# Kernel optimization log

Hardware: AMD Instinct MI355X
Metric: run time of the kernel (lower is better)

## Reference

```python
import jax, jax.numpy as jnp
import numpy as np

NEG_INF = -1e30

def setup_inputs() -> dict:
    key = jax.random.key(0)
    k1, k2, k3 = jax.random.split(key, 3)
    B, H, S, D = 2, 16, 2048, 128
    q = jax.random.normal(k1, (B, H, S, D), dtype=jnp.float32)
    k = jax.random.normal(k2, (B, H, S, D), dtype=jnp.float32)
    v = jax.random.normal(k3, (B, H, S, D), dtype=jnp.float32)
    return {"q": q, "k": k, "v": v}

def reference(q, k, v):
    # F.scaled_dot_product_attention(q, k, v, is_causal=True), MATH backend:
    # full score matrix, causal mask (top-left aligned: j <= i), softmax, bmm.
    D = q.shape[-1]
    scale = 1.0 / jnp.sqrt(jnp.asarray(D, dtype=q.dtype))
    scores = jnp.einsum('bhqd,bhkd->bhqk', q, k) * scale  # [B,H,S,S]
    Sq, Sk = scores.shape[-2], scores.shape[-1]
    causal = jnp.arange(Sk)[None, :] <= jnp.arange(Sq)[:, None]  # [Sq,Sk]
    scores = jnp.where(causal[None, None], scores, NEG_INF)
    attn = jax.nn.softmax(scores, axis=-1)
    return jnp.einsum('bhqk,bhkd->bhqd', attn, v)
```

## Files before the change

### kernel.cpp

```cpp
#include <hip/hip_runtime.h>
#include <cstdint>
#include <cstddef>

typedef __attribute__((ext_vector_type(8))) short short8;
typedef __attribute__((ext_vector_type(4))) float floatx4;
typedef __attribute__((ext_vector_type(2))) unsigned int uint2v;

namespace {
constexpr int kBH  = 32;
constexpr int kS   = 2048;
constexpr int kD   = 128;
constexpr int kBQ  = 64;
constexpr int kBK  = 64;
constexpr int kNQT = kS / kBQ;
constexpr int PST  = 72;
constexpr size_t kKVElems = (size_t)kBH * kS * kD;
}

__device__ __forceinline__ unsigned short f32_bf16(float f) {
    union { float f; unsigned u; } c; c.f = f;
    unsigned u = c.u;
    u += 0x7FFFu + ((u >> 16) & 1u);
    return (unsigned short)(u >> 16);
}

__device__ __forceinline__ unsigned pack_bf16x2(float lo, float hi) {
    return (unsigned)f32_bf16(lo) | ((unsigned)f32_bf16(hi) << 16);
}

__device__ __forceinline__ void gl_lds16(const void* g, void* l) {
    __builtin_amdgcn_global_load_lds(
        (const __attribute__((address_space(1))) unsigned int*)g,
        (__attribute__((address_space(3))) unsigned int*)l, 16, 0, 0);
}

__global__ __launch_bounds__(256)
void prepass(const float* __restrict__ K, const float* __restrict__ V,
             unsigned short* __restrict__ Kb, unsigned short* __restrict__ Vt) {
    const int b = (int)blockIdx.x;
    const int t = (int)threadIdx.x;
    if (b < 4096) {
        const size_t i0 = ((size_t)b * 256 + t) * 8;
        floatx4 a = *(const floatx4*)(K + i0);
        floatx4 c = *(const floatx4*)(K + i0 + 4);
        union { unsigned short us[8]; short8 v; } pk;
#pragma unroll
        for (int i = 0; i < 4; ++i) { pk.us[i] = f32_bf16(a[i]); pk.us[4 + i] = f32_bf16(c[i]); }
        *(short8*)(Kb + i0) = pk.v;
    } else {
        __shared__ float ldsT[64][68];
        const int vb = b - 4096;
        const int bh = vb >> 6;
        const int rem = vb & 63;
        const int s0 = (rem >> 1) * 64;
        const int d0 = (rem & 1) * 64;
        const float* vbase = V + ((size_t)bh * kS + s0) * kD + d0;
        const int sr = t >> 4, c4 = (t & 15) * 4;
#pragma unroll
        for (int p = 0; p < 4; ++p) {
            const int s = p * 16 + sr;
            *(floatx4*)&ldsT[s][c4] = *(const floatx4*)(vbase + (size_t)s * kD + c4);
        }
        __syncthreads();
        const int dr = t >> 2, sc = (t & 3) * 16;
        union { unsigned short us[16]; short8 v[2]; } pk;
#pragma unroll
        for (int j = 0; j < 16; ++j) pk.us[j] = f32_bf16(ldsT[sc + j][dr]);
        unsigned short* out = Vt + ((size_t)(bh * kD + d0 + dr)) * kS + s0 + sc;
        *(short8*)out = pk.v[0];
        *(short8*)(out + 8) = pk.v[1];
    }
}


struct TileState {
    short8  qf[4];
    floatx4 oacc[8];
    float   lsum[4];
};

__device__ __forceinline__ void tile_step(
    TileState& ts, const unsigned short* kT, const unsigned short* vT,
    unsigned short* pw, int l16, int quad, int rowl, bool doMask)
{
    floatx4 sacc[4];
#pragma unroll
    for (int nt = 0; nt < 4; ++nt) {
        floatx4 acc = (floatx4){0.f, 0.f, 0.f, 0.f};
#pragma unroll
        for (int ks = 0; ks < 4; ++ks) {
            short8 kf = *(const short8*)&kT[(nt * 16 + l16) * 128 + (((ks * 4 + quad) ^ l16) << 3)];
            acc = __builtin_amdgcn_mfma_f32_16x16x32_bf16(ts.qf[ks], kf, acc, 0, 0, 0);
        }
        sacc[nt] = acc;
    }

    if (doMask) {
#pragma unroll
        for (int nt = 0; nt < 4; ++nt) {
            const int col = nt * 16 + l16;
#pragma unroll
            for (int r = 0; r < 4; ++r)
                if (col > rowl + r) sacc[nt][r] = -1e30f;
        }
    }

#pragma unroll
    for (int nt = 0; nt < 4; ++nt)
#pragma unroll
        for (int r = 0; r < 4; ++r)
            sacc[nt][r] = __expf(sacc[nt][r]);
#pragma unroll
    for (int r = 0; r < 4; ++r)
        ts.lsum[r] += (sacc[0][r] + sacc[1][r]) + (sacc[2][r] + sacc[3][r]);

#pragma unroll
    for (int nt = 0; nt < 4; ++nt)
#pragma unroll
        for (int r = 0; r < 4; ++r)
            pw[(quad * 4 + r) * PST + nt * 16 + l16] = f32_bf16(sacc[nt][r]);

    short8 pf[2];
#pragma unroll
    for (int ks = 0; ks < 2; ++ks)
        pf[ks] = *(const short8*)&pw[l16 * PST + ks * 32 + quad * 8];

#pragma unroll
    for (int nd = 0; nd < 8; ++nd) {
        floatx4 acc = ts.oacc[nd];
#pragma unroll
        for (int ks = 0; ks < 2; ++ks) {
            short8 vf = *(const short8*)&vT[(nd * 16 + l16) * 64 + ((((ks * 4 + quad)) ^ (l16 & 7)) << 3)];
            acc = __builtin_amdgcn_mfma_f32_16x16x32_bf16(pf[ks], vf, acc, 0, 0, 0);
        }
        ts.oacc[nd] = acc;
    }
}

__global__ __launch_bounds__(256, 2)
void fa_fwd_ws(const float* __restrict__ Qg, const unsigned short* __restrict__ Kb,
               const unsigned short* __restrict__ Vt, float* __restrict__ Og) {
    const int id = (int)blockIdx.x;
    const int qA = id >> 5;
    const int qB = kNQT - 1 - qA;
    const int bh = id & (kBH - 1);
    const int t    = (int)threadIdx.x;
    const int wave = t >> 6;
    const int lane = t & 63;
    const int quad = lane >> 4;
    const int l16  = lane & 15;
    const int rowl = wave * 16 + quad * 4;

    __shared__ __align__(16) unsigned short kT0[kBK * 128];
    __shared__ __align__(16) unsigned short kT1[kBK * 128];
    __shared__ __align__(16) unsigned short vT0[kD * 64];
    __shared__ __align__(16) unsigned short vT1[kD * 64];
    __shared__ __align__(16) unsigned short pT[4 * 16 * PST];
    unsigned short* pw = &pT[wave * 16 * PST];

    const float scale = 0.08838834764831845f;

    TileState A, B;
#pragma unroll
    for (int i = 0; i < 8; ++i) { A.oacc[i] = (floatx4){0,0,0,0}; B.oacc[i] = (floatx4){0,0,0,0}; }
#pragma unroll
    for (int r = 0; r < 4; ++r) { A.lsum[r] = 0.f; B.lsum[r] = 0.f; }

    {
        const float* qpA = Qg + ((size_t)bh * kS + qA * kBQ + wave * 16 + l16) * kD;
        const float* qpB = Qg + ((size_t)bh * kS + qB * kBQ + wave * 16 + l16) * kD;
#pragma unroll
        for (int ks = 0; ks < 4; ++ks) {
            const int d0 = ks * 32 + quad * 8;
            floatx4 a0 = *(const floatx4*)(qpA + d0);
            floatx4 a1 = *(const floatx4*)(qpA + d0 + 4);
            floatx4 b0 = *(const floatx4*)(qpB + d0);
            floatx4 b1 = *(const floatx4*)(qpB + d0 + 4);
            union { unsigned short us[8]; short8 v; } pa, pb;
#pragma unroll
            for (int i = 0; i < 4; ++i) {
                pa.us[i]     = f32_bf16(a0[i] * scale);
                pa.us[4 + i] = f32_bf16(a1[i] * scale);
                pb.us[i]     = f32_bf16(b0[i] * scale);
                pb.us[4 + i] = f32_bf16(b1[i] * scale);
            }
            A.qf[ks] = pa.v;
            B.qf[ks] = pb.v;
        }
    }

    const unsigned short* kBase = Kb + (size_t)bh * kS * kD;
    const unsigned short* vBase = Vt + (size_t)bh * kD * kS;

    auto stage = [&](int kt, unsigned short* kDst, unsigned short* vDst) {
        const int kj0 = kt * kBK;
        const int rbase = wave * 16;
#pragma unroll
        for (int i = 0; i < 4; ++i) {
            const int row = rbase + i * 4 + (lane >> 4);
            const int cg  = (lane & 15) ^ (row & 15);
            gl_lds16(kBase + ((size_t)(kj0 + row)) * kD + cg * 8,
                     &kDst[(rbase + i * 4) * 128]);
        }
        const int dbase = wave * 32;
#pragma unroll
        for (int i = 0; i < 4; ++i) {
            const int d  = dbase + i * 8 + (lane >> 3);
            const int cg = (lane & 7) ^ (d & 7);
            gl_lds16(vBase + (size_t)d * kS + kj0 + cg * 8,
                     &vDst[(dbase + i * 8) * 64]);
        }
    };

    const int last = qB;
    stage(0, kT0, vT0);
    __syncthreads();

    int kt = 0;
    for (;;) {
        if (kt < last) stage(kt + 1, kT1, vT1);
        if (kt <= qA) tile_step(A, kT0, vT0, pw, l16, quad, rowl, kt == qA);
        tile_step(B, kT0, vT0, pw, l16, quad, rowl, kt == last);
        __syncthreads();
        if (kt == last) break;
        ++kt;
        if (kt < last) stage(kt + 1, kT0, vT0);
        if (kt <= qA) tile_step(A, kT1, vT1, pw, l16, quad, rowl, kt == qA);
        tile_step(B, kT1, vT1, pw, l16, quad, rowl, kt == last);
        __syncthreads();
        if (kt == last) break;
        ++kt;
    }

#pragma unroll
    for (int tile = 0; tile < 2; ++tile) {
        TileState& ts = tile ? B : A;
        const int qt = tile ? qB : qA;
        float ls[4];
#pragma unroll
        for (int r = 0; r < 4; ++r) ls[r] = ts.lsum[r];
#pragma unroll
        for (int off = 1; off < 16; off <<= 1)
#pragma unroll
            for (int r = 0; r < 4; ++r)
                ls[r] += __shfl_xor(ls[r], off, 64);
        float inv[4];
#pragma unroll
        for (int r = 0; r < 4; ++r) inv[r] = 1.0f / ls[r];
        float* ob = Og + ((size_t)bh * kS + qt * kBQ + wave * 16 + quad * 4) * kD;
#pragma unroll
        for (int nd = 0; nd < 8; ++nd)
#pragma unroll
            for (int r = 0; r < 4; ++r)
                ob[(size_t)r * kD + nd * 16 + l16] = ts.oacc[nd][r] * inv[r];
    }
}

namespace {
constexpr int KSTf = 136;
constexpr int VSTf = 72;
}

__device__ __forceinline__ void tile_step_f(
    TileState& ts, const unsigned short* kT, const unsigned short* vT,
    unsigned short* pw, int l16, int quad, int rowl, bool doMask)
{
    floatx4 sacc[4];
#pragma unroll
    for (int nt = 0; nt < 4; ++nt) {
        floatx4 acc = (floatx4){0.f, 0.f, 0.f, 0.f};
#pragma unroll
        for (int ks = 0; ks < 4; ++ks) {
            short8 kf = *(const short8*)&kT[(nt * 16 + l16) * KSTf + ks * 32 + quad * 8];
            acc = __builtin_amdgcn_mfma_f32_16x16x32_bf16(ts.qf[ks], kf, acc, 0, 0, 0);
        }
        sacc[nt] = acc;
    }
    if (doMask) {
#pragma unroll
        for (int nt = 0; nt < 4; ++nt) {
            const int col = nt * 16 + l16;
#pragma unroll
            for (int r = 0; r < 4; ++r)
                if (col > rowl + r) sacc[nt][r] = -1e30f;
        }
    }
#pragma unroll
    for (int nt = 0; nt < 4; ++nt)
#pragma unroll
        for (int r = 0; r < 4; ++r)
            sacc[nt][r] = __expf(sacc[nt][r]);
#pragma unroll
    for (int r = 0; r < 4; ++r)
        ts.lsum[r] += (sacc[0][r] + sacc[1][r]) + (sacc[2][r] + sacc[3][r]);
#pragma unroll
    for (int nt = 0; nt < 4; ++nt)
#pragma unroll
        for (int r = 0; r < 4; ++r)
            pw[(quad * 4 + r) * PST + nt * 16 + l16] = f32_bf16(sacc[nt][r]);
    short8 pf[2];
#pragma unroll
    for (int ks = 0; ks < 2; ++ks)
        pf[ks] = *(const short8*)&pw[l16 * PST + ks * 32 + quad * 8];
#pragma unroll
    for (int nd = 0; nd < 8; ++nd) {
        floatx4 acc = ts.oacc[nd];
#pragma unroll
        for (int ks = 0; ks < 2; ++ks) {
            short8 vf = *(const short8*)&vT[(nd * 16 + l16) * VSTf + ks * 32 + quad * 8];
            acc = __builtin_amdgcn_mfma_f32_16x16x32_bf16(pf[ks], vf, acc, 0, 0, 0);
        }
        ts.oacc[nd] = acc;
    }
}

__global__ __launch_bounds__(256, 2)
void fa_fwd_fallback(const float* __restrict__ Qg, const float* __restrict__ Kg,
                     const float* __restrict__ Vg, float* __restrict__ Og) {
    const int id = (int)blockIdx.x;
    const int qA = id >> 5;
    const int qB = kNQT - 1 - qA;
    const int bh = id & (kBH - 1);
    const int t    = (int)threadIdx.x;
    const int wave = t >> 6;
    const int lane = t & 63;
    const int quad = lane >> 4;
    const int l16  = lane & 15;
    const int rowl = wave * 16 + quad * 4;

    __shared__ __align__(16) unsigned short kT[2][kBK * KSTf];
    __shared__ __align__(16) unsigned short vT[2][kD * VSTf];
    __shared__ __align__(16) unsigned short pT[4 * 16 * PST];
    unsigned short* pw = &pT[wave * 16 * PST];

    const float scale = 0.08838834764831845f;

    TileState A, B;
#pragma unroll
    for (int i = 0; i < 8; ++i) { A.oacc[i] = (floatx4){0,0,0,0}; B.oacc[i] = (floatx4){0,0,0,0}; }
#pragma unroll
    for (int r = 0; r < 4; ++r) { A.lsum[r] = 0.f; B.lsum[r] = 0.f; }
    {
        const float* qpA = Qg + ((size_t)bh * kS + qA * kBQ + wave * 16 + l16) * kD;
        const float* qpB = Qg + ((size_t)bh * kS + qB * kBQ + wave * 16 + l16) * kD;
#pragma unroll
        for (int ks = 0; ks < 4; ++ks) {
            const int d0 = ks * 32 + quad * 8;
            floatx4 a0 = *(const floatx4*)(qpA + d0);
            floatx4 a1 = *(const floatx4*)(qpA + d0 + 4);
            floatx4 b0 = *(const floatx4*)(qpB + d0);
            floatx4 b1 = *(const floatx4*)(qpB + d0 + 4);
            union { unsigned short us[8]; short8 v; } pa, pb;
#pragma unroll
            for (int i = 0; i < 4; ++i) {
                pa.us[i]     = f32_bf16(a0[i] * scale);
                pa.us[4 + i] = f32_bf16(a1[i] * scale);
                pb.us[i]     = f32_bf16(b0[i] * scale);
                pb.us[4 + i] = f32_bf16(b1[i] * scale);
            }
            A.qf[ks] = pa.v;
            B.qf[ks] = pb.v;
        }
    }

    const int kRow8 = t >> 5;
    const int kCol4 = t & 31;
    const int vD    = t & 127;
    const int vR2   = t >> 7;
    const float* kBaseH = Kg + (size_t)bh * kS * kD;
    const float* vBaseH = Vg + (size_t)bh * kS * kD;
    floatx4 kpre[8];
    float   vpreL[16], vpreH[16];

    auto issue_kv_loads = [&](int kt) {
        const float* kb = kBaseH + (size_t)(kt * kBK) * kD;
        const float* vb = vBaseH + (size_t)(kt * kBK) * kD;
#pragma unroll
        for (int p = 0; p < 8; ++p)
            kpre[p] = *(const floatx4*)(kb + (size_t)(p * 8 + kRow8) * kD + kCol4 * 4);
#pragma unroll
        for (int p = 0; p < 16; ++p) {
            const int j = p * 2 + vR2;
            vpreL[p] = vb[(size_t)(2 * j) * kD + vD];
            vpreH[p] = vb[(size_t)(2 * j + 1) * kD + vD];
        }
    };
    auto store_kv = [&](int buf) {
#pragma unroll
        for (int p = 0; p < 8; ++p) {
            union { unsigned short us[4]; uint2v v; } w;
#pragma unroll
            for (int i = 0; i < 4; ++i) w.us[i] = f32_bf16(kpre[p][i]);
            *(uint2v*)&kT[buf][(p * 8 + kRow8) * KSTf + kCol4 * 4] = w.v;
        }
#pragma unroll
        for (int p = 0; p < 16; ++p) {
            const int j = p * 2 + vR2;
            *(unsigned*)&vT[buf][vD * VSTf + 2 * j] = pack_bf16x2(vpreL[p], vpreH[p]);
        }
    };

    const int last = qB;
    issue_kv_loads(0);
    store_kv(0);
    __syncthreads();
    for (int kt = 0; kt <= last; ++kt) {
        const int buf = kt & 1;
        if (kt < last) issue_kv_loads(kt + 1);
        if (kt <= qA) tile_step_f(A, kT[buf], vT[buf], pw, l16, quad, rowl, kt == qA);
        tile_step_f(B, kT[buf], vT[buf], pw, l16, quad, rowl, kt == last);
        if (kt < last) {
            store_kv(buf ^ 1);
            __syncthreads();
        }
    }
#pragma unroll
    for (int tile = 0; tile < 2; ++tile) {
        TileState& ts = tile ? B : A;
        const int qt = tile ? qB : qA;
        float ls[4];
#pragma unroll
        for (int r = 0; r < 4; ++r) ls[r] = ts.lsum[r];
#pragma unroll
        for (int off = 1; off < 16; off <<= 1)
#pragma unroll
            for (int r = 0; r < 4; ++r)
                ls[r] += __shfl_xor(ls[r], off, 64);
        float inv[4];
#pragma unroll
        for (int r = 0; r < 4; ++r) inv[r] = 1.0f / ls[r];
        float* ob = Og + ((size_t)bh * kS + qt * kBQ + wave * 16 + quad * 4) * kD;
#pragma unroll
        for (int nd = 0; nd < 8; ++nd)
#pragma unroll
            for (int r = 0; r < 4; ++r)
                ob[(size_t)r * kD + nd * 16 + l16] = ts.oacc[nd][r] * inv[r];
    }
}

extern "C" void kernel_launch(void* const* d_in, const int* in_sizes, int n_in,
                              void* d_out, int out_size, void* d_ws, size_t ws_size,
                              hipStream_t stream) {
    (void)in_sizes; (void)n_in; (void)out_size;
    const float* q = (const float*)d_in[0];
    const float* k = (const float*)d_in[1];
    const float* v = (const float*)d_in[2];
    float* o = (float*)d_out;
    const size_t need = 2 * kKVElems * sizeof(unsigned short);
    if (ws_size >= need) {
        unsigned short* Kb = (unsigned short*)d_ws;
        unsigned short* Vt = Kb + kKVElems;
        prepass<<<dim3(4096 + 2048), 256, 0, stream>>>(k, v, Kb, Vt);
        fa_fwd_ws<<<dim3((kNQT / 2) * kBH), 256, 0, stream>>>(q, Kb, Vt, o);
    } else {
        fa_fwd_fallback<<<dim3((kNQT / 2) * kBH), 256, 0, stream>>>(q, k, v, o);
    }
}
```

Baseline: 182.4 us.

## Single-buffer K/V staging, fold log2e into Q scale, swizzle P tile

Removes the K/V LDS double buffer in the main kernel. Each tile is now loaded and then synced before compute, which halves LDS use and may allow more resident blocks but gives up the overlap of loads with compute. The log2(e) factor is folded into the Q scale so the softmax can call exp2f instead of __expf. The P staging buffer changes from a padded stride of 72 to an XOR-swizzled stride of 64 to avoid LDS bank conflicts with less padding.

```diff
diff --git a/kernel.cpp b/kernel.cpp
--- a/kernel.cpp
+++ b/kernel.cpp
@@ -13,8 +13,8 @@
 constexpr int kBQ  = 64;
 constexpr int kBK  = 64;
 constexpr int kNQT = kS / kBQ;
-constexpr int PST  = 72;
 constexpr size_t kKVElems = (size_t)kBH * kS * kD;
+constexpr float kScale = 0.08838834764831845f * 1.44269504088896340736f;
 }
 
 __device__ __forceinline__ unsigned short f32_bf16(float f) {
@@ -109,7 +109,7 @@
     for (int nt = 0; nt < 4; ++nt)
 #pragma unroll
         for (int r = 0; r < 4; ++r)
-            sacc[nt][r] = __expf(sacc[nt][r]);
+            sacc[nt][r] = exp2f(sacc[nt][r]);
 #pragma unroll
     for (int r = 0; r < 4; ++r)
         ts.lsum[r] += (sacc[0][r] + sacc[1][r]) + (sacc[2][r] + sacc[3][r]);
@@ -117,20 +117,23 @@
 #pragma unroll
     for (int nt = 0; nt < 4; ++nt)
 #pragma unroll
-        for (int r = 0; r < 4; ++r)
-            pw[(quad * 4 + r) * PST + nt * 16 + l16] = f32_bf16(sacc[nt][r]);
+        for (int r = 0; r < 4; ++r) {
+            const int row = quad * 4 + r;
+            const int ch  = ((nt << 1) | (l16 >> 3)) ^ (row & 7);
+            pw[row * 64 + (ch << 3) + (l16 & 7)] = f32_bf16(sacc[nt][r]);
+        }
 
     short8 pf[2];
 #pragma unroll
     for (int ks = 0; ks < 2; ++ks)
-        pf[ks] = *(const short8*)&pw[l16 * PST + ks * 32 + quad * 8];
+        pf[ks] = *(const short8*)&pw[l16 * 64 + (((ks * 4 + quad) ^ (l16 & 7)) << 3)];
 
 #pragma unroll
     for (int nd = 0; nd < 8; ++nd) {
         floatx4 acc = ts.oacc[nd];
 #pragma unroll
         for (int ks = 0; ks < 2; ++ks) {
-            short8 vf = *(const short8*)&vT[(nd * 16 + l16) * 64 + ((((ks * 4 + quad)) ^ (l16 & 7)) << 3)];
+            short8 vf = *(const short8*)&vT[(nd * 16 + l16) * 64 + (((ks * 4 + quad) ^ (l16 & 7)) << 3)];
             acc = __builtin_amdgcn_mfma_f32_16x16x32_bf16(pf[ks], vf, acc, 0, 0, 0);
         }
         ts.oacc[nd] = acc;
@@ -151,14 +154,10 @@
     const int l16  = lane & 15;
     const int rowl = wave * 16 + quad * 4;
 
-    __shared__ __align__(16) unsigned short kT0[kBK * 128];
-    __shared__ __align__(16) unsigned short kT1[kBK * 128];
-    __shared__ __align__(16) unsigned short vT0[kD * 64];
-    __shared__ __align__(16) unsigned short vT1[kD * 64];
-    __shared__ __align__(16) unsigned short pT[4 * 16 * PST];
-    unsigned short* pw = &pT[wave * 16 * PST];
-
-    const float scale = 0.08838834764831845f;
+    __shared__ __align__(16) unsigned short kT[kBK * 128];
+    __shared__ __align__(16) unsigned short vT[kD * 64];
+    __shared__ __align__(16) unsigned short pT[4 * 16 * 64];
+    unsigned short* pw = &pT[wave * 16 * 64];
 
     TileState A, B;
 #pragma unroll
@@ -179,10 +178,10 @@
             union { unsigned short us[8]; short8 v; } pa, pb;
 #pragma unroll
             for (int i = 0; i < 4; ++i) {
-                pa.us[i]     = f32_bf16(a0[i] * scale);
-                pa.us[4 + i] = f32_bf16(a1[i] * scale);
-                pb.us[i]     = f32_bf16(b0[i] * scale);
-                pb.us[4 + i] = f32_bf16(b1[i] * scale);
+                pa.us[i]     = f32_bf16(a0[i] * kScale);
+                pa.us[4 + i] = f32_bf16(a1[i] * kScale);
+                pb.us[i]     = f32_bf16(b0[i] * kScale);
+                pb.us[4 + i] = f32_bf16(b1[i] * kScale);
             }
             A.qf[ks] = pa.v;
             B.qf[ks] = pb.v;
@@ -192,7 +191,7 @@
     const unsigned short* kBase = Kb + (size_t)bh * kS * kD;
     const unsigned short* vBase = Vt + (size_t)bh * kD * kS;
 
-    auto stage = [&](int kt, unsigned short* kDst, unsigned short* vDst) {
+    auto stage = [&](int kt) {
         const int kj0 = kt * kBK;
         const int rbase = wave * 16;
 #pragma unroll
@@ -200,7 +199,7 @@
             const int row = rbase + i * 4 + (lane >> 4);
             const int cg  = (lane & 15) ^ (row & 15);
             gl_lds16(kBase + ((size_t)(kj0 + row)) * kD + cg * 8,
-                     &kDst[(rbase + i * 4) * 128]);
+                     &kT[(rbase + i * 4) * 128]);
         }
         const int dbase = wave * 32;
 #pragma unroll
@@ -208,28 +207,17 @@
             const int d  = dbase + i * 8 + (lane >> 3);
             const int cg = (lane & 7) ^ (d & 7);
             gl_lds16(vBase + (size_t)d * kS + kj0 + cg * 8,
-                     &vDst[(dbase + i * 8) * 64]);
+                     &vT[(dbase + i * 8) * 64]);
         }
     };
 
     const int last = qB;
-    stage(0, kT0, vT0);
-    __syncthreads();
-
-    int kt = 0;
-    for (;;) {
-        if (kt < last) stage(kt + 1, kT1, vT1);
-        if (kt <= qA) tile_step(A, kT0, vT0, pw, l16, quad, rowl, kt == qA);
-        tile_step(B, kT0, vT0, pw, l16, quad, rowl, kt == last);
+    for (int kt = 0; kt <= last; ++kt) {
+        stage(kt);
         __syncthreads();
-        if (kt == last) break;
-        ++kt;
-        if (kt < last) stage(kt + 1, kT0, vT0);
-        if (kt <= qA) tile_step(A, kT1, vT1, pw, l16, quad, rowl, kt == qA);
-        tile_step(B, kT1, vT1, pw, l16, quad, rowl, kt == last);
+        if (kt <= qA) tile_step(A, kT, vT, pw, l16, quad, rowl, kt == qA);
+        tile_step(B, kT, vT, pw, l16, quad, rowl, kt == last);
         __syncthreads();
-        if (kt == last) break;
-        ++kt;
     }
 
 #pragma unroll
@@ -259,6 +247,7 @@
 namespace {
 constexpr int KSTf = 136;
 constexpr int VSTf = 72;
+constexpr int PSTf = 72;
 }
 
 __device__ __forceinline__ void tile_step_f(
@@ -289,7 +278,7 @@
     for (int nt = 0; nt < 4; ++nt)
 #pragma unroll
         for (int r = 0; r < 4; ++r)
-            sacc[nt][r] = __expf(sacc[nt][r]);
+            sacc[nt][r] = exp2f(sacc[nt][r]);
 #pragma unroll
     for (int r = 0; r < 4; ++r)
         ts.lsum[r] += (sacc[0][r] + sacc[1][r]) + (sacc[2][r] + sacc[3][r]);
@@ -297,11 +286,11 @@
     for (int nt = 0; nt < 4; ++nt)
 #pragma unroll
         for (int r = 0; r < 4; ++r)
-            pw[(quad * 4 + r) * PST + nt * 16 + l16] = f32_bf16(sacc[nt][r]);
+            pw[(quad * 4 + r) * PSTf + nt * 16 + l16] = f32_bf16(sacc[nt][r]);
     short8 pf[2];
 #pragma unroll
     for (int ks = 0; ks < 2; ++ks)
-        pf[ks] = *(const short8*)&pw[l16 * PST + ks * 32 + quad * 8];
+        pf[ks] = *(const short8*)&pw[l16 * PSTf + ks * 32 + quad * 8];
 #pragma unroll
     for (int nd = 0; nd < 8; ++nd) {
         floatx4 acc = ts.oacc[nd];
@@ -330,10 +319,8 @@
 
     __shared__ __align__(16) unsigned short kT[2][kBK * KSTf];
     __shared__ __align__(16) unsigned short vT[2][kD * VSTf];
-    __shared__ __align__(16) unsigned short pT[4 * 16 * PST];
-    unsigned short* pw = &pT[wave * 16 * PST];
-
-    const float scale = 0.08838834764831845f;
+    __shared__ __align__(16) unsigned short pT[4 * 16 * PSTf];
+    unsigned short* pw = &pT[wave * 16 * PSTf];
 
     TileState A, B;
 #pragma unroll
@@ -353,10 +340,10 @@
             union { unsigned short us[8]; short8 v; } pa, pb;
 #pragma unroll
             for (int i = 0; i < 4; ++i) {
-                pa.us[i]     = f32_bf16(a0[i] * scale);
-                pa.us[4 + i] = f32_bf16(a1[i] * scale);
-                pb.us[i]     = f32_bf16(b0[i] * scale);
-                pb.us[4 + i] = f32_bf16(b1[i] * scale);
+                pa.us[i]     = f32_bf16(a0[i] * kScale);
+                pa.us[4 + i] = f32_bf16(a1[i] * kScale);
+                pb.us[i]     = f32_bf16(b0[i] * kScale);
+                pb.us[4 + i] = f32_bf16(b1[i] * kScale);
             }
             A.qf[ks] = pa.v;
             B.qf[ks] = pb.v;
```

After: 189.8 us. 1.04x slower.
